# Performance work log

Measured on AMD Instinct MI355X. Metric: run time of the kernel, lower is better.

The kernel has to match this reference:

```python
import jax, jax.numpy as jnp
import numpy as np

J = 4                              # wavelet decomposition levels (level[i] = 4 for all experts)
PERM = (0, 1, 2, 3, 4, 5, 4, 5)    # original forward reuses experts 4,5 for gate slots 6,7 (repo bug, kept)


def haar_dwt(x):
    """One level of orthonormal 2D Haar DWT. x: [B,C,H,W] -> (ll [B,C,H/2,W/2], details [B,C,3,H/2,W/2])."""
    x00 = x[..., 0::2, 0::2]
    x01 = x[..., 0::2, 1::2]
    x10 = x[..., 1::2, 0::2]
    x11 = x[..., 1::2, 1::2]
    ll = (x00 + x01 + x10 + x11) * 0.5
    lh = (x00 + x01 - x10 - x11) * 0.5
    hl = (x00 - x01 + x10 - x11) * 0.5
    hh = (x00 - x01 - x10 + x11) * 0.5
    return ll, jnp.stack([lh, hl, hh], axis=2)


def haar_idwt(ll, h):
    """Inverse of haar_dwt. ll: [B,C,m,m], h: [B,C,3,m,m] -> [B,C,2m,2m]."""
    lh, hl, hh = h[:, :, 0], h[:, :, 1], h[:, :, 2]
    x00 = (ll + lh + hl + hh) * 0.5
    x01 = (ll + lh - hl - hh) * 0.5
    x10 = (ll - lh + hl - hh) * 0.5
    x11 = (ll - lh - hl + hh) * 0.5
    B, C, m, _ = ll.shape
    out = jnp.zeros((B, C, 2 * m, 2 * m), ll.dtype)
    out = out.at[..., 0::2, 0::2].set(x00)
    out = out.at[..., 0::2, 1::2].set(x01)
    out = out.at[..., 1::2, 0::2].set(x10)
    out = out.at[..., 1::2, 1::2].set(x11)
    return out


def _expert(x, wl, wh):
    """One WaveConv2d expert: J-level DWT, dense per-mode channel mixing of the coarsest
    approx (wl: [Ci,Co,m,m]) and the 3 coarsest detail bands (wh: [3,Ci,Co,m,m]),
    pass-through of finer detail levels, then inverse DWT."""
    highs = []
    for _ in range(J):
        x, h = haar_dwt(x)
        highs.append(h)
    x = jnp.einsum('bixy,ioxy->boxy', x, wl)
    highs[-1] = jnp.einsum('bikxy,kioxy->bokxy', highs[-1], wh)
    for h in reversed(highs):
        x = haar_idwt(x, h)
    return x


def setup_inputs() -> dict:
    key = jax.random.key(0)
    kx, kl, kw1, kw2 = jax.random.split(key, 4)
    B, C, S = 32, 64, 64
    m = S >> J                       # coarsest-level mode count = 4
    scale = 1.0 / (C * C)
    x = jax.random.normal(kx, (B, C, S, S), jnp.float32)
    lambda_ = jax.random.uniform(kl, (B, 1, 8, 1), dtype=jnp.float32)
    WL = scale * jax.random.uniform(kw1, (8, C, C, m, m), dtype=jnp.float32)
    WH = scale * jax.random.uniform(kw2, (8, 3, C, C, m, m), dtype=jnp.float32)
    return {"x": x, "lambda_": lambda_, "WL": WL, "WH": WH}


def reference(x, lambda_, WL, WH):
    # Only experts 0..5 are ever called by the original forward (6,7 are dead params).
    ys = jax.vmap(_expert, in_axes=(None, 0, 0))(x, WL[:6], WH[:6])   # [6,B,C,H,W]
    ys = ys[jnp.asarray(PERM)]                                        # [8,B,C,H,W]
    gate = jnp.moveaxis(lambda_, 2, 0)[..., None]                     # [8,B,1,1,1]
    return jnp.sum(gate * ys, axis=0)                                 # [B,C,H,W]
```

## Files before the change

kernel.cpp:

```cpp
#include <hip/hip_runtime.h>


#define COEF_N 131072
#define DELTA_N (4 * COEF_N)

typedef float floatx4 __attribute__((ext_vector_type(4)));

__global__ __launch_bounds__(256) void kA(const float* __restrict__ x,
                                          const float* __restrict__ WL,
                                          const float* __restrict__ WH,
                                          float* __restrict__ coef,
                                          float* __restrict__ wpack2) {
  int bi = blockIdx.x;
  int tid = threadIdx.x;
  if (bi < 512) {
    int b = bi >> 4;
    int cg = bi & 15;
    int wave = tid >> 6;
    int lane = tid & 63;
    int c = cg * 4 + wave;
    const float4* img4 = (const float4*)(x + (size_t)(b * 64 + c) * 4096);
    int col4 = lane & 15;
    int rgrp = lane >> 4;
    float top[4] = {0.f, 0.f, 0.f, 0.f}, bot[4] = {0.f, 0.f, 0.f, 0.f};
#pragma unroll
    for (int t = 0; t < 16; ++t) {
      int row = t * 4 + rgrp;
      float4 v = img4[row * 16 + col4];
      float s = v.x + v.y + v.z + v.w;
      if ((t & 3) < 2) top[t >> 2] += s;
      else             bot[t >> 2] += s;
    }
    float sc = ((col4 & 3) < 2) ? 1.0f : -1.0f;
    int Y = col4 >> 2;
#pragma unroll
    for (int X = 0; X < 4; ++X) {
      float s = top[X] + bot[X];
      float d = top[X] - bot[X];
      float r[4];
      r[0] = s; r[1] = d; r[2] = sc * s; r[3] = sc * d;
#pragma unroll
      for (int band = 0; band < 4; ++band) {
        float v = r[band];
        v += __shfl_xor(v, 1, 64);
        v += __shfl_xor(v, 2, 64);
        v += __shfl_xor(v, 16, 64);
        v += __shfl_xor(v, 32, 64);
        if ((lane & 3) == 0 && rgrp == 0) {
          coef[(((band * 4 + X) * 4 + Y) * 32 + b) * 64 + c] = v * 0.0625f;
        }
      }
    }
  } else {
    int gid = (bi - 512) * 256 + tid;
    int o = gid & 63;
    int i = (gid >> 6) & 63;
    int be = gid >> 12;
    int e = be % 6;
    int band = be / 6;
    const float* src;
    if (band == 0) src = WL + (size_t)((e * 64 + i) * 64 + o) * 16;
    else           src = WH + (size_t)(((e * 3 + (band - 1)) * 64 + i) * 64 + o) * 16;
    const float4* s4 = (const float4*)src;
    float4 v0 = s4[0], v1 = s4[1], v2 = s4[2], v3 = s4[3];
    float vv[16] = {v0.x, v0.y, v0.z, v0.w, v1.x, v1.y, v1.z, v1.w,
                    v2.x, v2.y, v2.z, v2.w, v3.x, v3.y, v3.z, v3.w};
    int ei = e * 64 + i;
    int eg = ei >> 2, er = ei & 3;
#pragma unroll
    for (int xy = 0; xy < 16; ++xy) {
      int bxy = band * 16 + xy;
      wpack2[(((size_t)bxy * 96 + eg) * 64 + o) * 4 + er] = vv[xy];
    }
  }
}

__global__ __launch_bounds__(512) void kB(const float* __restrict__ coef,
                                          const float* __restrict__ wpack2,
                                          const float* __restrict__ lam,
                                          float* __restrict__ delta) {
  __shared__ float4 Agv[96][8];
  __shared__ float rawA[32][65];
  __shared__ float gg[32][8];
  int blk = blockIdx.x;
  int bxy = blk >> 2;
  int q = blk & 3;
  int tid = threadIdx.x;
  const float* cslab = coef + (size_t)bxy * 2048;
  for (int idx = tid; idx < 2048; idx += 512) rawA[idx >> 6][idx & 63] = cslab[idx];
  if (tid < 32) {
    int b = tid;
    float l[8];
#pragma unroll
    for (int j = 0; j < 8; ++j) l[j] = lam[b * 8 + j];
    gg[b][0] = l[0]; gg[b][1] = l[1]; gg[b][2] = l[2]; gg[b][3] = l[3];
    gg[b][4] = l[4] + l[6];
    gg[b][5] = l[5] + l[7];
    gg[b][6] = l[0] + l[1] + l[2] + l[3] + l[4] + l[5] + l[6] + l[7];
  }
  __syncthreads();
  for (int idx = tid; idx < 96 * 8; idx += 512) {
    int eil = idx >> 3, bq = idx & 7;
    int ei = q * 96 + eil;
    int e = ei >> 6, i = ei & 63;
    float4 a;
    a.x = gg[bq * 4 + 0][e] * rawA[bq * 4 + 0][i];
    a.y = gg[bq * 4 + 1][e] * rawA[bq * 4 + 1][i];
    a.z = gg[bq * 4 + 2][e] * rawA[bq * 4 + 2][i];
    a.w = gg[bq * 4 + 3][e] * rawA[bq * 4 + 3][i];
    Agv[eil][bq] = a;
  }
  __syncthreads();
  int o = tid & 63;
  int bq = tid >> 6;
  const float4* wp = (const float4*)wpack2 + (size_t)bxy * (96 * 64) +
                     (size_t)(q * 24) * 64 + o;
  float acc0 = 0.f, acc1 = 0.f, acc2 = 0.f, acc3 = 0.f;
  for (int eg = 0; eg < 24; ++eg) {
    float4 w = wp[(size_t)eg * 64];
    float4 a0 = Agv[eg * 4 + 0][bq];
    float4 a1 = Agv[eg * 4 + 1][bq];
    float4 a2 = Agv[eg * 4 + 2][bq];
    float4 a3 = Agv[eg * 4 + 3][bq];
    acc0 += a0.x * w.x + a1.x * w.y + a2.x * w.z + a3.x * w.w;
    acc1 += a0.y * w.x + a1.y * w.y + a2.y * w.z + a3.y * w.w;
    acc2 += a0.z * w.x + a1.z * w.y + a2.z * w.z + a3.z * w.w;
    acc3 += a0.w * w.x + a1.w * w.y + a2.w * w.z + a3.w * w.w;
  }
  float* dslab = delta + (size_t)(q * 64 + bxy) * 2048;
  if (q == 0) {
    float G0 = gg[bq * 4 + 0][6], G1 = gg[bq * 4 + 1][6];
    float G2 = gg[bq * 4 + 2][6], G3 = gg[bq * 4 + 3][6];
    dslab[(bq * 4 + 0) * 64 + o] = acc0 - G0 * rawA[bq * 4 + 0][o];
    dslab[(bq * 4 + 1) * 64 + o] = acc1 - G1 * rawA[bq * 4 + 1][o];
    dslab[(bq * 4 + 2) * 64 + o] = acc2 - G2 * rawA[bq * 4 + 2][o];
    dslab[(bq * 4 + 3) * 64 + o] = acc3 - G3 * rawA[bq * 4 + 3][o];
  } else {
    dslab[(bq * 4 + 0) * 64 + o] = acc0;
    dslab[(bq * 4 + 1) * 64 + o] = acc1;
    dslab[(bq * 4 + 2) * 64 + o] = acc2;
    dslab[(bq * 4 + 3) * 64 + o] = acc3;
  }
}

__global__ __launch_bounds__(256) void kC(const float* __restrict__ x,
                                          const float* __restrict__ delta,
                                          const float* __restrict__ lam,
                                          float* __restrict__ out) {
  int bo = blockIdx.x;
  int b = bo >> 6, o = bo & 63;
  int tid = threadIdx.x;
  __shared__ float ds[64];
  if (tid < 64) {
    int band = tid >> 4, xy = tid & 15;
    float s = 0.f;
#pragma unroll
    for (int q = 0; q < 4; ++q) {
      s += delta[((size_t)(q * 64 + band * 16 + xy) * 32 + b) * 64 + o];
    }
    ds[tid] = s;
  }
  __syncthreads();
  float G = 0.f;
#pragma unroll
  for (int j = 0; j < 8; ++j) G += lam[b * 8 + j];
  int w4 = tid & 15;
  int h0 = tid >> 4;
  int Y = w4 >> 2;
  float sc = ((w4 & 3) < 2) ? 1.f : -1.f;
  float sr = (h0 < 8) ? 1.f : -1.f;
  const float4* xi = (const float4*)(x + (size_t)bo * 4096);
  floatx4* oi = (floatx4*)(out + (size_t)bo * 4096);
#pragma unroll
  for (int X = 0; X < 4; ++X) {
    float dsel = (ds[X * 4 + Y] + sr * ds[16 + X * 4 + Y] +
                  sc * ds[32 + X * 4 + Y] + sr * sc * ds[48 + X * 4 + Y]) * 0.0625f;
    int idx = (X * 16 + h0) * 16 + w4;
    float4 v = xi[idx];
    floatx4 r;
    r.x = G * v.x + dsel;
    r.y = G * v.y + dsel;
    r.z = G * v.z + dsel;
    r.w = G * v.w + dsel;
    __builtin_nontemporal_store(r, &oi[idx]);
  }
}

extern "C" void kernel_launch(void* const* d_in, const int* in_sizes, int n_in,
                              void* d_out, int out_size, void* d_ws, size_t ws_size,
                              hipStream_t stream) {
  const float* x   = (const float*)d_in[0];
  const float* lam = (const float*)d_in[1];
  const float* WL  = (const float*)d_in[2];
  const float* WH  = (const float*)d_in[3];
  float* out = (float*)d_out;
  float* coef   = (float*)d_ws;
  float* delta  = coef + COEF_N;
  float* wpack2 = delta + DELTA_N;

  hipLaunchKernelGGL(kA, dim3(896), dim3(256), 0, stream, x, WL, WH, coef, wpack2);
  hipLaunchKernelGGL(kB, dim3(256), dim3(512), 0, stream, coef, wpack2, lam, delta);
  hipLaunchKernelGGL(kC, dim3(2048), dim3(256), 0, stream, x, delta, lam, out);
}
```

Measured before the change: 107.9 us.

## Fuse three kernels into one cooperative kernel with grid syncs and register-held input

Merges the DWT-coefficient, weight-pack, channel-mixing and output kernels into one cooperative launch of 512 blocks separated by two grid-wide barriers. Each thread keeps its slice of the input image in registers from the first phase and reuses it for the final output, so x is not read from global memory a second time. The mixing phase is split into half-batch blocks to fill the 512-block grid. The aim is to remove two launch gaps and one full pass over x. The cost is grid-sync overhead, higher register pressure from holding 16 float4 per thread, and a hard requirement that all 512 blocks be co-resident.

```diff
diff --git a/kernel.cpp b/kernel.cpp
--- a/kernel.cpp
+++ b/kernel.cpp
@@ -1,4 +1,7 @@
 #include <hip/hip_runtime.h>
+#include <hip/hip_cooperative_groups.h>
+
+namespace cg = cooperative_groups;
 
 
 #define COEF_N 131072
@@ -6,53 +9,60 @@
 
 typedef float floatx4 __attribute__((ext_vector_type(4)));
 
-__global__ __launch_bounds__(256) void kA(const float* __restrict__ x,
-                                          const float* __restrict__ WL,
-                                          const float* __restrict__ WH,
-                                          float* __restrict__ coef,
-                                          float* __restrict__ wpack2) {
-  int bi = blockIdx.x;
+__global__ __launch_bounds__(256, 2) void kFused(
+    const float* __restrict__ x, const float* __restrict__ WL,
+    const float* __restrict__ WH, const float* __restrict__ lam,
+    float* __restrict__ coef, float* __restrict__ wpack2,
+    float* __restrict__ delta, float* __restrict__ out) {
+  __shared__ float gg[32][8];
+  __shared__ float4 Agv[96][4];
+  __shared__ float rawA[16][65];
+  __shared__ float dsL[4][64];
+
+  int blk = blockIdx.x;
   int tid = threadIdx.x;
-  if (bi < 512) {
-    int b = bi >> 4;
-    int cg = bi & 15;
-    int wave = tid >> 6;
-    int lane = tid & 63;
-    int c = cg * 4 + wave;
-    const float4* img4 = (const float4*)(x + (size_t)(b * 64 + c) * 4096);
-    int col4 = lane & 15;
-    int rgrp = lane >> 4;
-    float top[4] = {0.f, 0.f, 0.f, 0.f}, bot[4] = {0.f, 0.f, 0.f, 0.f};
+
+  int b = blk >> 4;
+  int cgi = blk & 15;
+  int wave = tid >> 6;
+  int lane = tid & 63;
+  int c = cgi * 4 + wave;
+  const float4* img4 = (const float4*)(x + (size_t)(b * 64 + c) * 4096);
+  int col4 = lane & 15;
+  int rgrp = lane >> 4;
+  float4 xr[16];
+  float top[4] = {0.f, 0.f, 0.f, 0.f}, bot[4] = {0.f, 0.f, 0.f, 0.f};
 #pragma unroll
-    for (int t = 0; t < 16; ++t) {
-      int row = t * 4 + rgrp;
-      float4 v = img4[row * 16 + col4];
-      float s = v.x + v.y + v.z + v.w;
-      if ((t & 3) < 2) top[t >> 2] += s;
-      else             bot[t >> 2] += s;
-    }
-    float sc = ((col4 & 3) < 2) ? 1.0f : -1.0f;
-    int Y = col4 >> 2;
+  for (int t = 0; t < 16; ++t) {
+    int row = t * 4 + rgrp;
+    float4 v = img4[row * 16 + col4];
+    xr[t] = v;
+    float s = v.x + v.y + v.z + v.w;
+    if ((t & 3) < 2) top[t >> 2] += s;
+    else             bot[t >> 2] += s;
+  }
+  float scn = ((col4 & 3) < 2) ? 1.0f : -1.0f;
+  int Yc = col4 >> 2;
 #pragma unroll
-    for (int X = 0; X < 4; ++X) {
-      float s = top[X] + bot[X];
-      float d = top[X] - bot[X];
-      float r[4];
-      r[0] = s; r[1] = d; r[2] = sc * s; r[3] = sc * d;
+  for (int X = 0; X < 4; ++X) {
+    float s = top[X] + bot[X];
+    float d = top[X] - bot[X];
+    float r[4];
+    r[0] = s; r[1] = d; r[2] = scn * s; r[3] = scn * d;
 #pragma unroll
-      for (int band = 0; band < 4; ++band) {
-        float v = r[band];
-        v += __shfl_xor(v, 1, 64);
-        v += __shfl_xor(v, 2, 64);
-        v += __shfl_xor(v, 16, 64);
-        v += __shfl_xor(v, 32, 64);
-        if ((lane & 3) == 0 && rgrp == 0) {
-          coef[(((band * 4 + X) * 4 + Y) * 32 + b) * 64 + c] = v * 0.0625f;
-        }
+    for (int band = 0; band < 4; ++band) {
+      float v = r[band];
+      v += __shfl_xor(v, 1, 64);
+      v += __shfl_xor(v, 2, 64);
+      v += __shfl_xor(v, 16, 64);
+      v += __shfl_xor(v, 32, 64);
+      if ((lane & 3) == 0 && rgrp == 0) {
+        coef[(((band * 4 + X) * 4 + Yc) * 32 + b) * 64 + c] = v * 0.0625f;
       }
     }
-  } else {
-    int gid = (bi - 512) * 256 + tid;
+  }
+  if (tid < 192) {
+    int gid = blk * 192 + tid;
     int o = gid & 63;
     int i = (gid >> 6) & 63;
     int be = gid >> 12;
@@ -73,116 +83,98 @@
       wpack2[(((size_t)bxy * 96 + eg) * 64 + o) * 4 + er] = vv[xy];
     }
   }
-}
+  cg::this_grid().sync();
 
-__global__ __launch_bounds__(512) void kB(const float* __restrict__ coef,
-                                          const float* __restrict__ wpack2,
-                                          const float* __restrict__ lam,
-                                          float* __restrict__ delta) {
-  __shared__ float4 Agv[96][8];
-  __shared__ float rawA[32][65];
-  __shared__ float gg[32][8];
-  int blk = blockIdx.x;
-  int bxy = blk >> 2;
-  int q = blk & 3;
-  int tid = threadIdx.x;
-  const float* cslab = coef + (size_t)bxy * 2048;
-  for (int idx = tid; idx < 2048; idx += 512) rawA[idx >> 6][idx & 63] = cslab[idx];
-  if (tid < 32) {
-    int b = tid;
-    float l[8];
+  {
+    int bxy = blk >> 3;
+    int q = (blk >> 1) & 3;
+    int h = blk & 1;
+    const float* cslab = coef + (size_t)bxy * 2048 + (size_t)h * 1024;
+    for (int idx = tid; idx < 1024; idx += 256)
+      rawA[idx >> 6][idx & 63] = cslab[idx];
+    if (tid < 32) {
+      int bb = tid;
+      float l[8];
 #pragma unroll
-    for (int j = 0; j < 8; ++j) l[j] = lam[b * 8 + j];
-    gg[b][0] = l[0]; gg[b][1] = l[1]; gg[b][2] = l[2]; gg[b][3] = l[3];
-    gg[b][4] = l[4] + l[6];
-    gg[b][5] = l[5] + l[7];
-    gg[b][6] = l[0] + l[1] + l[2] + l[3] + l[4] + l[5] + l[6] + l[7];
+      for (int j = 0; j < 8; ++j) l[j] = lam[bb * 8 + j];
+      gg[bb][0] = l[0]; gg[bb][1] = l[1]; gg[bb][2] = l[2]; gg[bb][3] = l[3];
+      gg[bb][4] = l[4] + l[6];
+      gg[bb][5] = l[5] + l[7];
+      gg[bb][6] = l[0] + l[1] + l[2] + l[3] + l[4] + l[5] + l[6] + l[7];
+    }
+    __syncthreads();
+    for (int idx = tid; idx < 96 * 4; idx += 256) {
+      int eil = idx >> 2, bql = idx & 3;
+      int ei = q * 96 + eil;
+      int e = ei >> 6, i = ei & 63;
+      int b0 = h * 16 + bql * 4;
+      float4 a;
+      a.x = gg[b0 + 0][e] * rawA[bql * 4 + 0][i];
+      a.y = gg[b0 + 1][e] * rawA[bql * 4 + 1][i];
+      a.z = gg[b0 + 2][e] * rawA[bql * 4 + 2][i];
+      a.w = gg[b0 + 3][e] * rawA[bql * 4 + 3][i];
+      Agv[eil][bql] = a;
+    }
+    __syncthreads();
+    int o = tid & 63;
+    int bql = tid >> 6;
+    const float4* wp = (const float4*)wpack2 + (size_t)bxy * (96 * 64) +
+                       (size_t)(q * 24) * 64 + o;
+    float acc0 = 0.f, acc1 = 0.f, acc2 = 0.f, acc3 = 0.f;
+    for (int eg = 0; eg < 24; ++eg) {
+      float4 w = wp[(size_t)eg * 64];
+      float4 a0 = Agv[eg * 4 + 0][bql];
+      float4 a1 = Agv[eg * 4 + 1][bql];
+      float4 a2 = Agv[eg * 4 + 2][bql];
+      float4 a3 = Agv[eg * 4 + 3][bql];
+      acc0 += a0.x * w.x + a1.x * w.y + a2.x * w.z + a3.x * w.w;
+      acc1 += a0.y * w.x + a1.y * w.y + a2.y * w.z + a3.y * w.w;
+      acc2 += a0.z * w.x + a1.z * w.y + a2.z * w.z + a3.z * w.w;
+      acc3 += a0.w * w.x + a1.w * w.y + a2.w * w.z + a3.w * w.w;
+    }
+    float* dslab = delta + (size_t)(q * 64 + bxy) * 2048;
+    int b0 = h * 16 + bql * 4;
+    if (q == 0) {
+      dslab[(b0 + 0) * 64 + o] = acc0 - gg[b0 + 0][6] * rawA[bql * 4 + 0][o];
+      dslab[(b0 + 1) * 64 + o] = acc1 - gg[b0 + 1][6] * rawA[bql * 4 + 1][o];
+      dslab[(b0 + 2) * 64 + o] = acc2 - gg[b0 + 2][6] * rawA[bql * 4 + 2][o];
+      dslab[(b0 + 3) * 64 + o] = acc3 - gg[b0 + 3][6] * rawA[bql * 4 + 3][o];
+    } else {
+      dslab[(b0 + 0) * 64 + o] = acc0;
+      dslab[(b0 + 1) * 64 + o] = acc1;
+      dslab[(b0 + 2) * 64 + o] = acc2;
+      dslab[(b0 + 3) * 64 + o] = acc3;
+    }
   }
-  __syncthreads();
-  for (int idx = tid; idx < 96 * 8; idx += 512) {
-    int eil = idx >> 3, bq = idx & 7;
-    int ei = q * 96 + eil;
-    int e = ei >> 6, i = ei & 63;
-    float4 a;
-    a.x = gg[bq * 4 + 0][e] * rawA[bq * 4 + 0][i];
-    a.y = gg[bq * 4 + 1][e] * rawA[bq * 4 + 1][i];
-    a.z = gg[bq * 4 + 2][e] * rawA[bq * 4 + 2][i];
-    a.w = gg[bq * 4 + 3][e] * rawA[bq * 4 + 3][i];
-    Agv[eil][bq] = a;
-  }
-  __syncthreads();
-  int o = tid & 63;
-  int bq = tid >> 6;
-  const float4* wp = (const float4*)wpack2 + (size_t)bxy * (96 * 64) +
-                     (size_t)(q * 24) * 64 + o;
-  float acc0 = 0.f, acc1 = 0.f, acc2 = 0.f, acc3 = 0.f;
-  for (int eg = 0; eg < 24; ++eg) {
-    float4 w = wp[(size_t)eg * 64];
-    float4 a0 = Agv[eg * 4 + 0][bq];
-    float4 a1 = Agv[eg * 4 + 1][bq];
-    float4 a2 = Agv[eg * 4 + 2][bq];
-    float4 a3 = Agv[eg * 4 + 3][bq];
-    acc0 += a0.x * w.x + a1.x * w.y + a2.x * w.z + a3.x * w.w;
-    acc1 += a0.y * w.x + a1.y * w.y + a2.y * w.z + a3.y * w.w;
-    acc2 += a0.z * w.x + a1.z * w.y + a2.z * w.z + a3.z * w.w;
-    acc3 += a0.w * w.x + a1.w * w.y + a2.w * w.z + a3.w * w.w;
-  }
-  float* dslab = delta + (size_t)(q * 64 + bxy) * 2048;
-  if (q == 0) {
-    float G0 = gg[bq * 4 + 0][6], G1 = gg[bq * 4 + 1][6];
-    float G2 = gg[bq * 4 + 2][6], G3 = gg[bq * 4 + 3][6];
-    dslab[(bq * 4 + 0) * 64 + o] = acc0 - G0 * rawA[bq * 4 + 0][o];
-    dslab[(bq * 4 + 1) * 64 + o] = acc1 - G1 * rawA[bq * 4 + 1][o];
-    dslab[(bq * 4 + 2) * 64 + o] = acc2 - G2 * rawA[bq * 4 + 2][o];
-    dslab[(bq * 4 + 3) * 64 + o] = acc3 - G3 * rawA[bq * 4 + 3][o];
-  } else {
-    dslab[(bq * 4 + 0) * 64 + o] = acc0;
-    dslab[(bq * 4 + 1) * 64 + o] = acc1;
-    dslab[(bq * 4 + 2) * 64 + o] = acc2;
-    dslab[(bq * 4 + 3) * 64 + o] = acc3;
-  }
-}
+  cg::this_grid().sync();
 
-__global__ __launch_bounds__(256) void kC(const float* __restrict__ x,
-                                          const float* __restrict__ delta,
-                                          const float* __restrict__ lam,
-                                          float* __restrict__ out) {
-  int bo = blockIdx.x;
-  int b = bo >> 6, o = bo & 63;
-  int tid = threadIdx.x;
-  __shared__ float ds[64];
-  if (tid < 64) {
-    int band = tid >> 4, xy = tid & 15;
+  {
+    int ch2 = tid >> 6;
+    int bxy2 = tid & 63;
+    int c2 = cgi * 4 + ch2;
     float s = 0.f;
 #pragma unroll
-    for (int q = 0; q < 4; ++q) {
-      s += delta[((size_t)(q * 64 + band * 16 + xy) * 32 + b) * 64 + o];
+    for (int q = 0; q < 4; ++q)
+      s += delta[((size_t)(q * 64 + bxy2) * 32 + b) * 64 + c2];
+    dsL[ch2][bxy2] = s;
+    __syncthreads();
+    float G = gg[b][6];
+    floatx4* oi = (floatx4*)(out + (size_t)(b * 64 + c) * 4096);
+#pragma unroll
+    for (int t = 0; t < 16; ++t) {
+      int X = t >> 2;
+      float sr = ((t & 3) < 2) ? 1.f : -1.f;
+      float dsel = (dsL[wave][X * 4 + Yc] + sr * dsL[wave][16 + X * 4 + Yc] +
+                    scn * dsL[wave][32 + X * 4 + Yc] +
+                    sr * scn * dsL[wave][48 + X * 4 + Yc]) * 0.0625f;
+      float4 v = xr[t];
+      floatx4 r;
+      r.x = G * v.x + dsel;
+      r.y = G * v.y + dsel;
+      r.z = G * v.z + dsel;
+      r.w = G * v.w + dsel;
+      __builtin_nontemporal_store(r, &oi[(t * 4 + rgrp) * 16 + col4]);
     }
-    ds[tid] = s;
-  }
-  __syncthreads();
-  float G = 0.f;
-#pragma unroll
-  for (int j = 0; j < 8; ++j) G += lam[b * 8 + j];
-  int w4 = tid & 15;
-  int h0 = tid >> 4;
-  int Y = w4 >> 2;
-  float sc = ((w4 & 3) < 2) ? 1.f : -1.f;
-  float sr = (h0 < 8) ? 1.f : -1.f;
-  const float4* xi = (const float4*)(x + (size_t)bo * 4096);
-  floatx4* oi = (floatx4*)(out + (size_t)bo * 4096);
-#pragma unroll
-  for (int X = 0; X < 4; ++X) {
-    float dsel = (ds[X * 4 + Y] + sr * ds[16 + X * 4 + Y] +
-                  sc * ds[32 + X * 4 + Y] + sr * sc * ds[48 + X * 4 + Y]) * 0.0625f;
-    int idx = (X * 16 + h0) * 16 + w4;
-    float4 v = xi[idx];
-    floatx4 r;
-    r.x = G * v.x + dsel;
-    r.y = G * v.y + dsel;
-    r.z = G * v.z + dsel;
-    r.w = G * v.w + dsel;
-    __builtin_nontemporal_store(r, &oi[idx]);
   }
 }
 
@@ -198,7 +190,7 @@
   float* delta  = coef + COEF_N;
   float* wpack2 = delta + DELTA_N;
 
-  hipLaunchKernelGGL(kA, dim3(896), dim3(256), 0, stream, x, WL, WH, coef, wpack2);
-  hipLaunchKernelGGL(kB, dim3(256), dim3(512), 0, stream, coef, wpack2, lam, delta);
-  hipLaunchKernelGGL(kC, dim3(2048), dim3(256), 0, stream, x, delta, lam, out);
+  void* args[] = {(void*)&x, (void*)&WL, (void*)&WH, (void*)&lam,
+                  (void*)&coef, (void*)&wpack2, (void*)&delta, (void*)&out};
+  hipLaunchCooperativeKernel((void*)kFused, dim3(512), dim3(256), args, 0, stream);
 }
```

Result: slower. 236.4 us (+119.1%).
